# Performance work log

Measured on AMD Instinct MI355X. Metric: run time of the kernel, lower is better.

## Reference

```python
import jax, jax.numpy as jnp
import numpy as np

D = 1024   # embedding_dim
H = 16     # head_num
DH = D // H
STD = 0.02


def setup_inputs() -> dict:
    key = jax.random.key(0)
    ks = jax.random.split(key, 8)
    B, S = 16, 2048
    inp = {
        "hidden_states": jax.random.normal(ks[0], (B, S, D), dtype=jnp.float32),
        "attention_mask": jnp.zeros((B, 1, S), dtype=jnp.float32),
        # nn.Linear params, stored as [in, out] for direct matmul
        "Wq": jax.random.normal(ks[1], (D, D), dtype=jnp.float32) * STD,
        "bq": jnp.zeros((D,), dtype=jnp.float32),
        "Wqa": jax.random.normal(ks[2], (D, H), dtype=jnp.float32) * STD,
        "bqa": jnp.zeros((H,), dtype=jnp.float32),
        "Wk": jax.random.normal(ks[3], (D, D), dtype=jnp.float32) * STD,
        "bk": jnp.zeros((D,), dtype=jnp.float32),
        "Wka": jax.random.normal(ks[4], (D, H), dtype=jnp.float32) * STD,
        "bka": jnp.zeros((H,), dtype=jnp.float32),
        "Wt": jax.random.normal(ks[5], (D, D), dtype=jnp.float32) * STD,
        "bt": jnp.zeros((D,), dtype=jnp.float32),
    }
    return inp


def reference(hidden_states, attention_mask, Wq, bq, Wqa, bqa, Wk, bk, Wka, bka, Wt, bt):
    B, S, _ = hidden_states.shape
    scale = 1.0 / np.sqrt(DH).astype(np.float32)

    mixed_q = hidden_states @ Wq + bq          # [B,S,D]
    mixed_k = hidden_states @ Wk + bk          # [B,S,D]

    # per-head query pooling scores: [B,S,H] -> [B,H,S]
    q_score = jnp.transpose(mixed_q @ Wqa + bqa, (0, 2, 1)) * scale + attention_mask
    q_weight = jax.nn.softmax(q_score, axis=-1)                 # [B,H,S]

    q_layer = mixed_q.reshape(B, S, H, DH).transpose(0, 2, 1, 3)  # [B,H,S,dh]
    pooled_q = jnp.einsum('bhs,bhsd->bhd', q_weight, q_layer)     # [B,H,dh]
    pooled_q_flat = pooled_q.reshape(B, 1, D)                     # [B,1,D] (head-major)

    # elementwise modulate keys with pooled query (broadcast, no repeat)
    mixed_qk = mixed_k * pooled_q_flat                            # [B,S,D]

    qk_score = jnp.transpose(mixed_qk @ Wka + bka, (0, 2, 1)) * scale + attention_mask
    qk_weight = jax.nn.softmax(qk_score, axis=-1)                 # [B,H,S]

    k_layer = mixed_qk.reshape(B, S, H, DH).transpose(0, 2, 1, 3)  # [B,H,S,dh]
    pooled_k = jnp.einsum('bhs,bhsd->bhd', qk_weight, k_layer)     # [B,H,dh]

    weighted = pooled_k[:, :, None, :] * q_layer                   # [B,H,S,dh]
    weighted = weighted.transpose(0, 2, 1, 3).reshape(B, S, D)     # [B,S,D]

    return weighted @ Wt + bt + mixed_q
```

## Files before the change

### kernel.cpp

```cpp
#include <hip/hip_runtime.h>
#include <hip/hip_bf16.h>
#include <stdint.h>

#define D_ 1024
#define H_ 16
#define DH_ 64
#define S_ 2048
#define B_ 16
static constexpr float SCALE = 0.125f;

typedef __bf16 bf16_t;
typedef __bf16 bf16x8 __attribute__((ext_vector_type(8)));
typedef __bf16 bf16x4 __attribute__((ext_vector_type(4)));
typedef float  f32x4  __attribute__((ext_vector_type(4)));

__device__ __forceinline__ void llds16(const void* g, void* l) {
  __builtin_amdgcn_global_load_lds(
      (const __attribute__((address_space(1))) void*)g,
      (__attribute__((address_space(3))) void*)l, 16, 0, 0);
}

__global__ __launch_bounds__(256)
void f32_to_bf16(const float* __restrict__ src, bf16_t* __restrict__ dst) {
  size_t base = ((size_t)blockIdx.x * 256 + threadIdx.x) * 8;
  f32x4 a = *(const f32x4*)&src[base];
  f32x4 b = *(const f32x4*)&src[base + 4];
  bf16x8 o;
#pragma unroll
  for (int i = 0; i < 4; ++i) { o[i] = (bf16_t)a[i]; o[4 + i] = (bf16_t)b[i]; }
  *(bf16x8*)&dst[base] = o;
}

__global__ __launch_bounds__(256)
void transpose1024(const float* __restrict__ src, bf16_t* __restrict__ dst) {
  __shared__ bf16_t t[64][65];
  const int n0 = blockIdx.x * 64, k0 = blockIdx.y * 64;
  const int r = threadIdx.x >> 4, c4 = (threadIdx.x & 15) * 4;
#pragma unroll
  for (int p = 0; p < 4; ++p) {
    int row = p * 16 + r;
    f32x4 f = *(const f32x4*)&src[(size_t)(k0 + row) * 1024 + n0 + c4];
#pragma unroll
    for (int i = 0; i < 4; ++i) t[row][c4 + i] = (bf16_t)f[i];
  }
  __syncthreads();
#pragma unroll
  for (int p = 0; p < 4; ++p) {
    int row = p * 16 + r;
    bf16x4 v;
#pragma unroll
    for (int i = 0; i < 4; ++i) v[i] = t[c4 + i][row];
    *(bf16x4*)&dst[(size_t)(n0 + row) * 1024 + k0 + c4] = v;
  }
}

__global__ __launch_bounds__(256)
void transpose_small(const float* __restrict__ src, bf16_t* __restrict__ dst) {
  int k = blockIdx.x * 256 + threadIdx.x;
  if (k < 1024) {
#pragma unroll
    for (int h = 0; h < H_; ++h) dst[h * 1024 + k] = (bf16_t)src[k * H_ + h];
  }
}

__global__ __launch_bounds__(256)
void conv_misc(const float* bq, const float* bk, const float* bt,
               const float* bqa, const float* bka, const float* mask,
               bf16_t* obq, bf16_t* obk, bf16_t* obt,
               bf16_t* obqa, bf16_t* obka, bf16_t* omask) {
  int i = blockIdx.x * 256 + threadIdx.x;
  const float* src; bf16_t* dst; int off;
  if      (i < 1024)  { src = bq;   dst = obq;   off = i; }
  else if (i < 2048)  { src = bk;   dst = obk;   off = i - 1024; }
  else if (i < 3072)  { src = bt;   dst = obt;   off = i - 2048; }
  else if (i < 3088)  { src = bqa;  dst = obqa;  off = i - 3072; }
  else if (i < 3104)  { src = bka;  dst = obka;  off = i - 3088; }
  else if (i < 35872) { src = mask; dst = omask; off = i - 3104; }
  else return;
  dst[off] = (bf16_t)src[off];
}

template <int MODE>
__global__ __launch_bounds__(256, 2)
void gemm_bt(const bf16_t* __restrict__ A, const bf16_t* __restrict__ BT,
             const bf16_t* __restrict__ bias, void* __restrict__ Cout,
             const float* __restrict__ pscale, const bf16_t* __restrict__ resid) {
  constexpr int K = 1024, N = 1024;
  __shared__ __align__(16) bf16_t lA[128 * 32];
  __shared__ __align__(16) bf16_t lB[128 * 32];
  const int tid = threadIdx.x;
  const int lane = tid & 63, wid = tid >> 6;
  const int wr = wid >> 1, wc = wid & 1;

  const int wgid = (blockIdx.x & 7) * 256 + (blockIdx.x >> 3);
  const int m0 = (wgid >> 3) * 128;
  const int n0 = (wgid & 7) * 128;

  const int ar = lane & 15;
  const int ak = (lane >> 4) * 8;

  f32x4 acc[4][4] = {};

  for (int k0 = 0; k0 < K; k0 += 32) {
#pragma unroll
    for (int j = 0; j < 2; ++j) {
      int c = j * 256 + tid;
      int row = c >> 2, kc = (c & 3) * 8;
      const bf16_t* ga = A + (size_t)(m0 + row) * K + k0 + kc;
      const bf16_t* gb = BT + (size_t)(n0 + row) * K + k0 + kc;
      bf16_t* la = lA + (size_t)(j * 256 + wid * 64) * 8;
      bf16_t* lb = lB + (size_t)(j * 256 + wid * 64) * 8;
      llds16(ga, la);
      llds16(gb, lb);
    }
    __syncthreads();
    bf16x8 af[4], bg[4];
#pragma unroll
    for (int m = 0; m < 4; ++m)
      af[m] = *(const bf16x8*)&lA[(wr * 64 + m * 16 + ar) * 32 + ak];
#pragma unroll
    for (int n = 0; n < 4; ++n)
      bg[n] = *(const bf16x8*)&lB[(wc * 64 + n * 16 + ar) * 32 + ak];
#pragma unroll
    for (int m = 0; m < 4; ++m)
#pragma unroll
      for (int n = 0; n < 4; ++n)
        acc[m][n] = __builtin_amdgcn_mfma_f32_16x16x32_bf16(af[m], bg[n], acc[m][n], 0, 0, 0);
    __syncthreads();
  }

  const int b = m0 / S_;
#pragma unroll
  for (int m = 0; m < 4; ++m) {
#pragma unroll
    for (int n = 0; n < 4; ++n) {
      const int col = n0 + wc * 64 + n * 16 + (lane & 15);
      const int row_base = m0 + wr * 64 + m * 16 + (lane >> 4) * 4;
      const float bcol = (float)bias[col];
      const float sc = (MODE == 1) ? pscale[b * D_ + col] : 1.0f;
#pragma unroll
      for (int j = 0; j < 4; ++j) {
        const int row = row_base + j;
        float v = acc[m][n][j] + bcol;
        if (MODE == 1) v *= sc;
        if (MODE == 2) {
          v += (float)resid[(size_t)row * N + col];
          ((float*)Cout)[(size_t)row * N + col] = v;
        } else {
          ((bf16_t*)Cout)[(size_t)row * N + col] = (bf16_t)v;
        }
      }
    }
  }
}

__global__ __launch_bounds__(256)
void score_kernel(const bf16_t* __restrict__ X, const bf16_t* __restrict__ WaT,
                  const bf16_t* __restrict__ ba, const bf16_t* __restrict__ mask,
                  float* __restrict__ scores) {
  const int lane = threadIdx.x & 63, wid = threadIdx.x >> 6;
  const int m0 = blockIdx.x * 64 + wid * 16;
  const int ar = lane & 15, ak = (lane >> 4) * 8;
  f32x4 acc = {};
  for (int k0 = 0; k0 < D_; k0 += 32) {
    bf16x8 a = *(const bf16x8*)&X[(size_t)(m0 + ar) * D_ + k0 + ak];
    bf16x8 b = *(const bf16x8*)&WaT[(size_t)ar * D_ + k0 + ak];
    acc = __builtin_amdgcn_mfma_f32_16x16x32_bf16(a, b, acc, 0, 0, 0);
  }
  const int h = lane & 15;
  const int srow = m0 + (lane >> 4) * 4;
  const int bb = srow / S_;
  const int s0 = srow - bb * S_;
  const float bah = (float)ba[h];
  f32x4 outv;
#pragma unroll
  for (int j = 0; j < 4; ++j)
    outv[j] = (acc[j] + bah) * SCALE + (float)mask[(size_t)bb * S_ + s0 + j];
  *(f32x4*)&scores[((size_t)(bb * H_ + h)) * S_ + s0] = outv;
}

__global__ __launch_bounds__(256)
void softmax_rows(const float* __restrict__ scores, float* __restrict__ wout) {
  __shared__ float rA[4], rB[4];
  const int tid = threadIdx.x, lane = tid & 63, wid = tid >> 6;
  const float* srow = scores + (size_t)blockIdx.x * S_;
  float* wrow = wout + (size_t)blockIdx.x * S_;
  f32x4 v0 = *(const f32x4*)&srow[tid * 4];
  f32x4 v1 = *(const f32x4*)&srow[1024 + tid * 4];
  float mx = fmaxf(fmaxf(fmaxf(v0[0], v0[1]), fmaxf(v0[2], v0[3])),
                   fmaxf(fmaxf(v1[0], v1[1]), fmaxf(v1[2], v1[3])));
#pragma unroll
  for (int o = 32; o; o >>= 1) mx = fmaxf(mx, __shfl_xor(mx, o));
  if (lane == 0) rA[wid] = mx;
  __syncthreads();
  mx = fmaxf(fmaxf(rA[0], rA[1]), fmaxf(rA[2], rA[3]));
  float sum = 0.f;
#pragma unroll
  for (int i = 0; i < 4; ++i) { v0[i] = __expf(v0[i] - mx); sum += v0[i]; }
#pragma unroll
  for (int i = 0; i < 4; ++i) { v1[i] = __expf(v1[i] - mx); sum += v1[i]; }
#pragma unroll
  for (int o = 32; o; o >>= 1) sum += __shfl_xor(sum, o);
  if (lane == 0) rB[wid] = sum;
  __syncthreads();
  sum = rB[0] + rB[1] + rB[2] + rB[3];
  const float inv = 1.0f / sum;
#pragma unroll
  for (int i = 0; i < 4; ++i) { v0[i] *= inv; v1[i] *= inv; }
  *(f32x4*)&wrow[tid * 4] = v0;
  *(f32x4*)&wrow[1024 + tid * 4] = v1;
}

__global__ __launch_bounds__(256)
void pool_partial(const bf16_t* __restrict__ X, const float* __restrict__ w,
                  float* __restrict__ partials) {
  __shared__ float sm[2][1024];
  const int tid = threadIdx.x;
  const int chunk = blockIdx.x, b = blockIdx.y;
  const int s0 = chunk * 32;
  const int dc = (tid & 127) * 8;
  const int sp = tid >> 7;
  const int h = dc >> 6;
  const float* wrow = w + ((size_t)b * H_ + h) * S_ + s0;
  const bf16_t* Xb = X + ((size_t)b * S_ + s0) * D_ + dc;
  float acc[8] = {};
  for (int s = sp; s < 32; s += 2) {
    bf16x8 xv = *(const bf16x8*)&Xb[(size_t)s * D_];
    float wt = wrow[s];
#pragma unroll
    for (int j = 0; j < 8; ++j) acc[j] += wt * (float)xv[j];
  }
#pragma unroll
  for (int j = 0; j < 8; ++j) sm[sp][dc + j] = acc[j];
  __syncthreads();
  const int d0 = tid * 4;
  f32x4 r;
#pragma unroll
  for (int j = 0; j < 4; ++j) r[j] = sm[0][d0 + j] + sm[1][d0 + j];
  *(f32x4*)&partials[((size_t)chunk * B_ + b) * D_ + d0] = r;
}

__global__ __launch_bounds__(256)
void pool_reduce(const float* __restrict__ partials, float* __restrict__ pooled) {
  const int idx = blockIdx.x * 256 + threadIdx.x;
  float s = 0.f;
#pragma unroll 8
  for (int c = 0; c < 64; ++c) s += partials[(size_t)c * (B_ * D_) + idx];
  pooled[idx] = s;
}

__global__ __launch_bounds__(256)
void weighted_kernel(const bf16_t* __restrict__ mq, const float* __restrict__ pk,
                     bf16_t* __restrict__ out) {
  size_t idx = ((size_t)blockIdx.x * 256 + threadIdx.x) * 8;
  int d0 = (int)(idx & (D_ - 1));
  int b = (int)(idx >> 21);
  bf16x8 v = *(const bf16x8*)&mq[idx];
  const float* pkb = pk + (size_t)b * D_ + d0;
  bf16x8 o;
#pragma unroll
  for (int i = 0; i < 8; ++i) o[i] = (bf16_t)((float)v[i] * pkb[i]);
  *(bf16x8*)&out[idx] = o;
}

extern "C" void kernel_launch(void* const* d_in, const int* in_sizes, int n_in,
                              void* d_out, int out_size, void* d_ws, size_t ws_size,
                              hipStream_t stream) {
  const float* hs   = (const float*)d_in[0];
  const float* mask = (const float*)d_in[1];
  const float* Wq   = (const float*)d_in[2];
  const float* bq   = (const float*)d_in[3];
  const float* Wqa  = (const float*)d_in[4];
  const float* bqa  = (const float*)d_in[5];
  const float* Wk   = (const float*)d_in[6];
  const float* bk   = (const float*)d_in[7];
  const float* Wka  = (const float*)d_in[8];
  const float* bka  = (const float*)d_in[9];
  const float* Wt   = (const float*)d_in[10];
  const float* bt   = (const float*)d_in[11];

  char* ws = (char*)d_ws;
  float*  pq    = (float*)(ws + (64u << 10));
  float*  pk    = (float*)(ws + (128u << 10));
  bf16_t* bqc   = (bf16_t*)(ws + (192u << 10));
  bf16_t* bkc   = (bf16_t*)(ws + (192u << 10) + 4096);
  bf16_t* btc   = (bf16_t*)(ws + (192u << 10) + 8192);
  bf16_t* bqac  = (bf16_t*)(ws + (192u << 10) + 12288);
  bf16_t* bkac  = (bf16_t*)(ws + (192u << 10) + 12352);
  bf16_t* maskc = (bf16_t*)(ws + (256u << 10));
  bf16_t* WqaT  = (bf16_t*)(ws + (1u << 20));
  bf16_t* WkaT  = (bf16_t*)(ws + (1u << 20) + 32768);
  bf16_t* WqT   = (bf16_t*)(ws + (2u << 20));
  bf16_t* WkT   = (bf16_t*)(ws + (4u << 20));
  bf16_t* WtT   = (bf16_t*)(ws + (6u << 20));
  bf16_t* hsb   = (bf16_t*)(ws + (8u << 20));
  bf16_t* mq    = (bf16_t*)(ws + (8u << 20) + ((size_t)64 << 20));
  bf16_t* mqk   = (bf16_t*)(ws + (8u << 20) + ((size_t)128 << 20));
  bf16_t* wtd   = (bf16_t*)(ws + (8u << 20) + ((size_t)192 << 20));
  float* scores = (float*)(ws + (8u << 20) + ((size_t)256 << 20));
  float* wsm    = (float*)(ws + (8u << 20) + ((size_t)258 << 20));
  float* parts  = (float*)(ws + (8u << 20) + ((size_t)260 << 20));

  f32_to_bf16<<<16384, 256, 0, stream>>>(hs, hsb);
  conv_misc<<<141, 256, 0, stream>>>(bq, bk, bt, bqa, bka, mask,
                                     bqc, bkc, btc, bqac, bkac, maskc);
  transpose1024<<<dim3(16, 16), 256, 0, stream>>>(Wq, WqT);
  transpose1024<<<dim3(16, 16), 256, 0, stream>>>(Wk, WkT);
  transpose1024<<<dim3(16, 16), 256, 0, stream>>>(Wt, WtT);
  transpose_small<<<4, 256, 0, stream>>>(Wqa, WqaT);
  transpose_small<<<4, 256, 0, stream>>>(Wka, WkaT);

  gemm_bt<0><<<2048, 256, 0, stream>>>(hsb, WqT, bqc, mq, nullptr, nullptr);

  score_kernel<<<512, 256, 0, stream>>>(mq, WqaT, bqac, maskc, scores);
  softmax_rows<<<256, 256, 0, stream>>>(scores, wsm);
  pool_partial<<<dim3(64, 16), 256, 0, stream>>>(mq, wsm, parts);
  pool_reduce<<<64, 256, 0, stream>>>(parts, pq);

  gemm_bt<1><<<2048, 256, 0, stream>>>(hsb, WkT, bkc, mqk, pq, nullptr);

  score_kernel<<<512, 256, 0, stream>>>(mqk, WkaT, bkac, maskc, scores);
  softmax_rows<<<256, 256, 0, stream>>>(scores, wsm);
  pool_partial<<<dim3(64, 16), 256, 0, stream>>>(mqk, wsm, parts);
  pool_reduce<<<64, 256, 0, stream>>>(parts, pk);

  weighted_kernel<<<16384, 256, 0, stream>>>(mq, pk, wtd);

  gemm_bt<2><<<2048, 256, 0, stream>>>(wtd, WtT, btc, d_out, nullptr, mq);
}
```

Measured before the change: 422.0 us.

## Replace GEMM with 256x256 double-buffered, LDS-swizzled kernel and staged epilogue

Replaces the 128x128, BK=32 single-buffered GEMM with a 256x256 tile, BK=64, 512-thread kernel. It double-buffers LDS via global_load_lds, using vmcnt waits, XOR-swizzled LDS rows and s_setprio around the MFMA blocks. The epilogue stages accumulators through LDS so it can do vectorized coalesced stores, and it reads fp32 biases directly, which removes their bf16 conversion. The aim is more data reuse per tile and overlap of loads with MFMA. The cost is 128KB of LDS per block and fewer blocks (512), which may hurt occupancy and tail balance.

```diff
diff --git a/kernel.cpp b/kernel.cpp
--- a/kernel.cpp
+++ b/kernel.cpp
@@ -64,92 +64,164 @@
 }
 
 __global__ __launch_bounds__(256)
-void conv_misc(const float* bq, const float* bk, const float* bt,
-               const float* bqa, const float* bka, const float* mask,
-               bf16_t* obq, bf16_t* obk, bf16_t* obt,
+void conv_misc(const float* bqa, const float* bka, const float* mask,
                bf16_t* obqa, bf16_t* obka, bf16_t* omask) {
   int i = blockIdx.x * 256 + threadIdx.x;
   const float* src; bf16_t* dst; int off;
-  if      (i < 1024)  { src = bq;   dst = obq;   off = i; }
-  else if (i < 2048)  { src = bk;   dst = obk;   off = i - 1024; }
-  else if (i < 3072)  { src = bt;   dst = obt;   off = i - 2048; }
-  else if (i < 3088)  { src = bqa;  dst = obqa;  off = i - 3072; }
-  else if (i < 3104)  { src = bka;  dst = obka;  off = i - 3088; }
-  else if (i < 35872) { src = mask; dst = omask; off = i - 3104; }
+  if      (i < 16)    { src = bqa;  dst = obqa;  off = i; }
+  else if (i < 32)    { src = bka;  dst = obka;  off = i - 16; }
+  else if (i < 32800) { src = mask; dst = omask; off = i - 32; }
   else return;
   dst[off] = (bf16_t)src[off];
 }
 
 template <int MODE>
-__global__ __launch_bounds__(256, 2)
-void gemm_bt(const bf16_t* __restrict__ A, const bf16_t* __restrict__ BT,
-             const bf16_t* __restrict__ bias, void* __restrict__ Cout,
+__global__ __launch_bounds__(512, 2)
+void gemm256(const bf16_t* __restrict__ A, const bf16_t* __restrict__ BT,
+             const float* __restrict__ bias, void* __restrict__ Cout,
              const float* __restrict__ pscale, const bf16_t* __restrict__ resid) {
-  constexpr int K = 1024, N = 1024;
-  __shared__ __align__(16) bf16_t lA[128 * 32];
-  __shared__ __align__(16) bf16_t lB[128 * 32];
+  constexpr int K = 1024;
+  __shared__ __align__(16) bf16_t lds[2][2][256 * 64];
   const int tid = threadIdx.x;
   const int lane = tid & 63, wid = tid >> 6;
-  const int wr = wid >> 1, wc = wid & 1;
-
-  const int wgid = (blockIdx.x & 7) * 256 + (blockIdx.x >> 3);
-  const int m0 = (wgid >> 3) * 128;
-  const int n0 = (wgid & 7) * 128;
-
+  const int wm = wid >> 2, wn = wid & 3;
+
+  const int wgid = (blockIdx.x & 7) * 64 + (blockIdx.x >> 3);
+  const int m0 = (wgid >> 2) * 256;
+  const int n0 = (wgid & 3) * 256;
+
+  const bf16_t* gA[4];
+  const bf16_t* gB[4];
+  int ldsOff[4];
+#pragma unroll
+  for (int i = 0; i < 4; ++i) {
+    int c = i * 512 + tid;
+    int r = c >> 3, j = c & 7;
+    int col = ((j ^ (r & 7)) << 3);
+    gA[i] = A  + (size_t)(m0 + r) * K + col;
+    gB[i] = BT + (size_t)(n0 + r) * K + col;
+    ldsOff[i] = c * 8;
+  }
+
+  f32x4 acc[8][4] = {};
   const int ar = lane & 15;
-  const int ak = (lane >> 4) * 8;
-
-  f32x4 acc[4][4] = {};
-
-  for (int k0 = 0; k0 < K; k0 += 32) {
-#pragma unroll
-    for (int j = 0; j < 2; ++j) {
-      int c = j * 256 + tid;
-      int row = c >> 2, kc = (c & 3) * 8;
-      const bf16_t* ga = A + (size_t)(m0 + row) * K + k0 + kc;
-      const bf16_t* gb = BT + (size_t)(n0 + row) * K + k0 + kc;
-      bf16_t* la = lA + (size_t)(j * 256 + wid * 64) * 8;
-      bf16_t* lb = lB + (size_t)(j * 256 + wid * 64) * 8;
-      llds16(ga, la);
-      llds16(gb, lb);
-    }
-    __syncthreads();
-    bf16x8 af[4], bg[4];
-#pragma unroll
-    for (int m = 0; m < 4; ++m)
-      af[m] = *(const bf16x8*)&lA[(wr * 64 + m * 16 + ar) * 32 + ak];
-#pragma unroll
-    for (int n = 0; n < 4; ++n)
-      bg[n] = *(const bf16x8*)&lB[(wc * 64 + n * 16 + ar) * 32 + ak];
-#pragma unroll
-    for (int m = 0; m < 4; ++m)
+  const int kq = lane >> 4;
+
+#pragma unroll
+  for (int i = 0; i < 4; ++i) { llds16(gA[i], &lds[0][0][ldsOff[i]]); llds16(gB[i], &lds[0][1][ldsOff[i]]); }
+#pragma unroll
+  for (int i = 0; i < 4; ++i) { llds16(gA[i] + 64, &lds[1][0][ldsOff[i]]); llds16(gB[i] + 64, &lds[1][1][ldsOff[i]]); }
+
+#pragma unroll 2
+  for (int t = 0; t < 16; ++t) {
+    const int cur = t & 1;
+    if (t < 15) asm volatile("s_waitcnt vmcnt(8)" ::: "memory");
+    else        asm volatile("s_waitcnt vmcnt(0)" ::: "memory");
+    __builtin_amdgcn_s_barrier();
+
+    const bf16_t* bufA = &lds[cur][0][0];
+    const bf16_t* bufB = &lds[cur][1][0];
+    bf16x8 af[8], bg[4];
+#pragma unroll
+    for (int m = 0; m < 8; ++m) {
+      int r = wm * 128 + m * 16 + ar;
+      af[m] = *(const bf16x8*)&bufA[r * 64 + (((kq) ^ (r & 7)) << 3)];
+    }
+#pragma unroll
+    for (int n = 0; n < 4; ++n) {
+      int r = wn * 64 + n * 16 + ar;
+      bg[n] = *(const bf16x8*)&bufB[r * 64 + (((kq) ^ (r & 7)) << 3)];
+    }
+    __builtin_amdgcn_s_setprio(1);
+#pragma unroll
+    for (int m = 0; m < 8; ++m)
 #pragma unroll
       for (int n = 0; n < 4; ++n)
         acc[m][n] = __builtin_amdgcn_mfma_f32_16x16x32_bf16(af[m], bg[n], acc[m][n], 0, 0, 0);
-    __syncthreads();
-  }
-
+    __builtin_amdgcn_s_setprio(0);
+#pragma unroll
+    for (int m = 0; m < 8; ++m) {
+      int r = wm * 128 + m * 16 + ar;
+      af[m] = *(const bf16x8*)&bufA[r * 64 + (((kq + 4) ^ (r & 7)) << 3)];
+    }
+#pragma unroll
+    for (int n = 0; n < 4; ++n) {
+      int r = wn * 64 + n * 16 + ar;
+      bg[n] = *(const bf16x8*)&bufB[r * 64 + (((kq + 4) ^ (r & 7)) << 3)];
+    }
+    asm volatile("s_waitcnt lgkmcnt(0)" ::: "memory");
+    __builtin_amdgcn_s_barrier();
+    if (t + 2 < 16) {
+      const int koff = (t + 2) * 64;
+      bf16_t* dA = &lds[cur][0][0];
+      bf16_t* dB = &lds[cur][1][0];
+#pragma unroll
+      for (int i = 0; i < 4; ++i) { llds16(gA[i] + koff, dA + ldsOff[i]); llds16(gB[i] + koff, dB + ldsOff[i]); }
+    }
+    __builtin_amdgcn_s_setprio(1);
+#pragma unroll
+    for (int m = 0; m < 8; ++m)
+#pragma unroll
+      for (int n = 0; n < 4; ++n)
+        acc[m][n] = __builtin_amdgcn_mfma_f32_16x16x32_bf16(af[m], bg[n], acc[m][n], 0, 0, 0);
+    __builtin_amdgcn_s_setprio(0);
+  }
+
+  float* st = (float*)(&lds[0][0][0]) + wid * (16 * 68);
   const int b = m0 / S_;
-#pragma unroll
-  for (int m = 0; m < 4; ++m) {
-#pragma unroll
-    for (int n = 0; n < 4; ++n) {
-      const int col = n0 + wc * 64 + n * 16 + (lane & 15);
-      const int row_base = m0 + wr * 64 + m * 16 + (lane >> 4) * 4;
-      const float bcol = (float)bias[col];
-      const float sc = (MODE == 1) ? pscale[b * D_ + col] : 1.0f;
-#pragma unroll
-      for (int j = 0; j < 4; ++j) {
-        const int row = row_base + j;
-        float v = acc[m][n][j] + bcol;
-        if (MODE == 1) v *= sc;
-        if (MODE == 2) {
-          v += (float)resid[(size_t)row * N + col];
-          ((float*)Cout)[(size_t)row * N + col] = v;
-        } else {
-          ((bf16_t*)Cout)[(size_t)row * N + col] = (bf16_t)v;
-        }
-      }
+  const int erow = lane >> 2;
+  const int ecol = (lane & 3) * 16;
+  const int gcb = n0 + wn * 64;
+  const int qrow = (lane >> 4) * 4;
+  const int qcol = lane & 15;
+  f32x4 bb[4], ps[4];
+#pragma unroll
+  for (int q = 0; q < 4; ++q) bb[q] = *(const f32x4*)&bias[gcb + ecol + q * 4];
+  if (MODE == 1) {
+#pragma unroll
+    for (int q = 0; q < 4; ++q) ps[q] = *(const f32x4*)&pscale[b * D_ + gcb + ecol + q * 4];
+  }
+#pragma unroll
+  for (int m = 0; m < 8; ++m) {
+#pragma unroll
+    for (int n = 0; n < 4; ++n)
+#pragma unroll
+      for (int j = 0; j < 4; ++j)
+        st[(qrow + j) * 68 + n * 16 + qcol] = acc[m][n][j];
+    asm volatile("s_waitcnt lgkmcnt(0)" ::: "memory");
+    const int grow = m0 + wm * 128 + m * 16 + erow;
+    f32x4 v[4];
+#pragma unroll
+    for (int q = 0; q < 4; ++q) v[q] = *(f32x4*)&st[erow * 68 + ecol + q * 4];
+#pragma unroll
+    for (int q = 0; q < 4; ++q)
+#pragma unroll
+      for (int i = 0; i < 4; ++i) v[q][i] += bb[q][i];
+    if (MODE == 1) {
+#pragma unroll
+      for (int q = 0; q < 4; ++q)
+#pragma unroll
+        for (int i = 0; i < 4; ++i) v[q][i] *= ps[q][i];
+    }
+    if (MODE == 2) {
+      bf16x8 r0 = *(const bf16x8*)&resid[(size_t)grow * D_ + gcb + ecol];
+      bf16x8 r1 = *(const bf16x8*)&resid[(size_t)grow * D_ + gcb + ecol + 8];
+#pragma unroll
+      for (int i = 0; i < 4; ++i) { v[0][i] += (float)r0[i]; v[1][i] += (float)r0[4 + i]; }
+#pragma unroll
+      for (int i = 0; i < 4; ++i) { v[2][i] += (float)r1[i]; v[3][i] += (float)r1[4 + i]; }
+      float* op = (float*)Cout + (size_t)grow * D_ + gcb + ecol;
+#pragma unroll
+      for (int q = 0; q < 4; ++q) *(f32x4*)&op[q * 4] = v[q];
+    } else {
+      bf16x8 o0, o1;
+#pragma unroll
+      for (int i = 0; i < 4; ++i) { o0[i] = (bf16_t)v[0][i]; o0[4 + i] = (bf16_t)v[1][i]; }
+#pragma unroll
+      for (int i = 0; i < 4; ++i) { o1[i] = (bf16_t)v[2][i]; o1[4 + i] = (bf16_t)v[3][i]; }
+      bf16_t* op = (bf16_t*)Cout + (size_t)grow * D_ + gcb + ecol;
+      *(bf16x8*)&op[0] = o0;
+      *(bf16x8*)&op[8] = o1;
     }
   }
 }
@@ -282,11 +354,8 @@
   char* ws = (char*)d_ws;
   float*  pq    = (float*)(ws + (64u << 10));
   float*  pk    = (float*)(ws + (128u << 10));
-  bf16_t* bqc   = (bf16_t*)(ws + (192u << 10));
-  bf16_t* bkc   = (bf16_t*)(ws + (192u << 10) + 4096);
-  bf16_t* btc   = (bf16_t*)(ws + (192u << 10) + 8192);
-  bf16_t* bqac  = (bf16_t*)(ws + (192u << 10) + 12288);
-  bf16_t* bkac  = (bf16_t*)(ws + (192u << 10) + 12352);
+  bf16_t* bqac  = (bf16_t*)(ws + (192u << 10));
+  bf16_t* bkac  = (bf16_t*)(ws + (192u << 10) + 64);
   bf16_t* maskc = (bf16_t*)(ws + (256u << 10));
   bf16_t* WqaT  = (bf16_t*)(ws + (1u << 20));
   bf16_t* WkaT  = (bf16_t*)(ws + (1u << 20) + 32768);
@@ -302,22 +371,21 @@
   float* parts  = (float*)(ws + (8u << 20) + ((size_t)260 << 20));
 
   f32_to_bf16<<<16384, 256, 0, stream>>>(hs, hsb);
-  conv_misc<<<141, 256, 0, stream>>>(bq, bk, bt, bqa, bka, mask,
-                                     bqc, bkc, btc, bqac, bkac, maskc);
+  conv_misc<<<129, 256, 0, stream>>>(bqa, bka, mask, bqac, bkac, maskc);
   transpose1024<<<dim3(16, 16), 256, 0, stream>>>(Wq, WqT);
   transpose1024<<<dim3(16, 16), 256, 0, stream>>>(Wk, WkT);
   transpose1024<<<dim3(16, 16), 256, 0, stream>>>(Wt, WtT);
   transpose_small<<<4, 256, 0, stream>>>(Wqa, WqaT);
   transpose_small<<<4, 256, 0, stream>>>(Wka, WkaT);
 
-  gemm_bt<0><<<2048, 256, 0, stream>>>(hsb, WqT, bqc, mq, nullptr, nullptr);
+  gemm256<0><<<512, 512, 0, stream>>>(hsb, WqT, bq, mq, nullptr, nullptr);
 
   score_kernel<<<512, 256, 0, stream>>>(mq, WqaT, bqac, maskc, scores);
   softmax_rows<<<256, 256, 0, stream>>>(scores, wsm);
   pool_partial<<<dim3(64, 16), 256, 0, stream>>>(mq, wsm, parts);
   pool_reduce<<<64, 256, 0, stream>>>(parts, pq);
 
-  gemm_bt<1><<<2048, 256, 0, stream>>>(hsb, WkT, bkc, mqk, pq, nullptr);
+  gemm256<1><<<512, 512, 0, stream>>>(hsb, WkT, bk, mqk, pq, nullptr);
 
   score_kernel<<<512, 256, 0, stream>>>(mqk, WkaT, bkac, maskc, scores);
   softmax_rows<<<256, 256, 0, stream>>>(scores, wsm);
@@ -326,5 +394,5 @@
 
   weighted_kernel<<<16384, 256, 0, stream>>>(mq, pk, wtd);
 
-  gemm_bt<2><<<2048, 256, 0, stream>>>(wtd, WtT, btc, d_out, nullptr, mq);
-}
+  gemm256<2><<<512, 512, 0, stream>>>(wtd, WtT, bt, d_out, nullptr, mq);
+}
```

Result: slower. 756.5 us (+79.3%).
